# Kernel tuning notes

Hardware: AMD Instinct MI355X
Metric: run time of the kernel (lower is better)

Reference implementation:

```python
import jax, jax.numpy as jnp
import numpy as np

B, N_LAT, N_PAT = 32, 64, 4096
DIM_LAT = DIM_PAT = DIM_ATTN = 192
H = 6
HD = DIM_ATTN // H  # 32
SCALE = HD ** -0.5


def setup_inputs() -> dict:
    key = jax.random.key(0)
    ks = jax.random.split(key, 8)
    s = lambda fan_in: 1.0 / np.sqrt(fan_in)
    return {
        "x_latents": jax.random.normal(ks[0], (B, N_LAT, DIM_LAT), jnp.float32),
        "x_patches": jax.random.normal(ks[1], (B, N_PAT, DIM_PAT), jnp.float32),
        # weights stored [in, out] (torch Linear applies x @ W.T; math identical)
        "W_rv_lat": jax.random.uniform(ks[2], (DIM_LAT, 2 * DIM_ATTN), jnp.float32, -s(DIM_LAT), s(DIM_LAT)),
        "W_rv_pat": jax.random.uniform(ks[3], (DIM_PAT, 2 * DIM_ATTN), jnp.float32, -s(DIM_PAT), s(DIM_PAT)),
        "W_proj_lat": jax.random.uniform(ks[4], (DIM_ATTN, DIM_LAT), jnp.float32, -s(DIM_ATTN), s(DIM_ATTN)),
        "b_proj_lat": jax.random.uniform(ks[5], (DIM_LAT,), jnp.float32, -s(DIM_ATTN), s(DIM_ATTN)),
        "W_proj_pat": jax.random.uniform(ks[6], (DIM_ATTN, DIM_PAT), jnp.float32, -s(DIM_ATTN), s(DIM_ATTN)),
        "b_proj_pat": jax.random.uniform(ks[7], (DIM_PAT,), jnp.float32, -s(DIM_ATTN), s(DIM_ATTN)),
    }


def _split_rv(x, W, n):
    # x: [B, n, d_in] -> r, v each [B, H, n, HD]
    rv = (x @ W).reshape(x.shape[0], n, 2, H, HD)
    rv = jnp.transpose(rv, (2, 0, 3, 1, 4))  # [2, B, H, n, HD]
    return rv[0], rv[1]


def reference(x_latents, x_patches, W_rv_lat, W_rv_pat,
              W_proj_lat, b_proj_lat, W_proj_pat, b_proj_pat):
    r_lat, v_lat = _split_rv(x_latents, W_rv_lat, N_LAT)   # [B,H,N_lat,HD]
    r_pat, v_pat = _split_rv(x_patches, W_rv_pat, N_PAT)   # [B,H,N_pat,HD]

    # single score matrix, softmaxed along both axes (dropout = 0, eval mode)
    scores = jnp.einsum('bhld,bhpd->bhlp', r_lat, r_pat) * SCALE  # [B,H,N_lat,N_pat]
    attn = jax.nn.softmax(scores, axis=-1)    # row-wise (over patches)
    attn_T = jax.nn.softmax(scores, axis=-2)  # col-wise (over latents)

    out_lat = jnp.einsum('bhlp,bhpd->blhd', attn, v_pat).reshape(B, N_LAT, DIM_ATTN)
    out_pat = jnp.einsum('bhlp,bhld->bphd', attn_T, v_lat).reshape(B, N_PAT, DIM_ATTN)

    out_lat = out_lat @ W_proj_lat + b_proj_lat
    out_pat = out_pat @ W_proj_pat + b_proj_pat
    return out_lat, out_pat
```

## Files before the change

kernel.cpp:

```cpp
#include <hip/hip_runtime.h>

#define B_   32
#define NL_  64
#define NP_  4096
#define DIM_ 192
#define H_   6
#define HD_  32
#define PC_  128
#define NCH_ (NP_/PC_)

typedef unsigned short u16;
typedef __attribute__((ext_vector_type(8))) short bf16x8;
typedef __attribute__((ext_vector_type(4))) short bf16x4;
typedef __attribute__((ext_vector_type(4))) float f32x4;

#define MFMA16(a,b,c) __builtin_amdgcn_mfma_f32_16x16x32_bf16(a,b,c,0,0,0)

__device__ __forceinline__ float bf2f(u16 s){ return __builtin_bit_cast(float,(unsigned)s<<16); }
__device__ __forceinline__ u16 f2bf(float f){
  unsigned u = __builtin_bit_cast(unsigned,f);
  return (u16)((u + 0x7FFFu + ((u>>16)&1u))>>16);
}

__global__ void k0_transpose(const float* __restrict__ W0, const float* __restrict__ W1,
                             const float* __restrict__ W2, const float* __restrict__ W3,
                             u16* __restrict__ T0, u16* __restrict__ T1,
                             u16* __restrict__ T2, u16* __restrict__ T3){
  int m = blockIdx.x >> 4, sub = blockIdx.x & 15;
  const float* src; u16* dst; int R, C;
  if      (m==0){src=W0;dst=T0;R=192;C=384;}
  else if (m==1){src=W1;dst=T1;R=192;C=384;}
  else if (m==2){src=W2;dst=T2;R=192;C=192;}
  else          {src=W3;dst=T3;R=192;C=192;}
  int total = R*C;
  for (int o = sub*256 + threadIdx.x; o < total; o += 16*256){
    int c = o / R, r = o - c*R;
    dst[o] = f2bf(src[r*C + c]);
  }
}

__global__ __launch_bounds__(256) void k_rv(const float* __restrict__ X,
    const u16* __restrict__ Wt, u16* __restrict__ R, u16* __restrict__ V,
    int Nseq, int nshift){
  __shared__ u16 As[64*200];
  __shared__ u16 Bs[64*200];
  const int t = threadIdx.x;
  const int m0 = blockIdx.x*64;
  const int lane = t & 63, w = t >> 6, g = lane >> 4, ln = lane & 15;
  const int wr = w >> 1, wc = w & 1;
  const int srow = t >> 2, sc = (t & 3) * 8;
  const f32x4 ZF = {0.f,0.f,0.f,0.f};

  #pragma unroll
  for (int k0 = 0; k0 < 192; k0 += 32){
    float4 x0 = *(const float4*)&X[(size_t)(m0 + srow)*192 + k0 + sc];
    float4 x1 = *(const float4*)&X[(size_t)(m0 + srow)*192 + k0 + sc + 4];
    bf16x8 av;
    av[0]=(short)f2bf(x0.x); av[1]=(short)f2bf(x0.y); av[2]=(short)f2bf(x0.z); av[3]=(short)f2bf(x0.w);
    av[4]=(short)f2bf(x1.x); av[5]=(short)f2bf(x1.y); av[6]=(short)f2bf(x1.z); av[7]=(short)f2bf(x1.w);
    *(bf16x8*)&As[srow*200 + k0 + sc] = av;
  }

  for (int n0 = 0; n0 < 384; n0 += 64){
    __syncthreads();
    #pragma unroll
    for (int k0 = 0; k0 < 192; k0 += 32)
      *(bf16x8*)&Bs[srow*200 + k0 + sc] = *(const bf16x8*)&Wt[(size_t)(n0 + srow)*192 + k0 + sc];
    __syncthreads();

    f32x4 acc[2][2];
    #pragma unroll
    for(int i=0;i<2;i++){ acc[i][0]=ZF; acc[i][1]=ZF; }
    #pragma unroll
    for (int k0 = 0; k0 < 192; k0 += 32){
      bf16x8 a0 = *(const bf16x8*)&As[(wr*32      + ln)*200 + k0 + g*8];
      bf16x8 a1 = *(const bf16x8*)&As[(wr*32 + 16 + ln)*200 + k0 + g*8];
      bf16x8 b0 = *(const bf16x8*)&Bs[(wc*32      + ln)*200 + k0 + g*8];
      bf16x8 b1 = *(const bf16x8*)&Bs[(wc*32 + 16 + ln)*200 + k0 + g*8];
      acc[0][0] = MFMA16(a0,b0,acc[0][0]);
      acc[0][1] = MFMA16(a0,b1,acc[0][1]);
      acc[1][0] = MFMA16(a1,b0,acc[1][0]);
      acc[1][1] = MFMA16(a1,b1,acc[1][1]);
    }
    #pragma unroll
    for(int i=0;i<2;i++)
      #pragma unroll
      for(int j=0;j<2;j++){
        int n = n0 + wc*32 + j*16 + ln;
        u16* dst; int c;
        if (n < 192){ dst = R; c = n; } else { dst = V; c = n - 192; }
        int h = c >> 5, d = c & 31;
        #pragma unroll
        for(int r=0;r<4;r++){
          int m = m0 + wr*32 + i*16 + g*4 + r;
          int b = m >> nshift, sidx = m & (Nseq-1);
          dst[((((size_t)b*H_ + h)*(size_t)Nseq + sidx) << 5) + d] = f2bf(acc[i][j][r]);
        }
      }
  }
}

__global__ __launch_bounds__(256) void k_attn(
    const u16* __restrict__ r_lat_g, const u16* __restrict__ v_lat_g,
    const u16* __restrict__ r_pat_g, const u16* __restrict__ v_pat_g,
    u16* __restrict__ Opat,
    float* __restrict__ numT_ws,
    float* __restrict__ rowsum_ws){
  const float SCALE = 0.17677669529663687f;
  const int ci = blockIdx.x, h = blockIdx.y, b = blockIdx.z;
  const int bh = b*H_ + h;
  const int t = threadIdx.x, lane = t&63, w = t>>6, g = lane>>4, ln = lane&15;
  __shared__ u16 RL [64*40];
  __shared__ u16 VLT[32*72];
  __shared__ u16 EN [128*72];
  __shared__ u16 ET [64*136];
  __shared__ float RS[4*64];
  __shared__ u16 POOL[128*40];
  u16* RP  = POOL;
  u16* VPT = POOL;
  const f32x4 ZF = {0.f,0.f,0.f,0.f};

  const size_t latbase = (size_t)bh * (NL_*HD_);
  { int row = t>>2, col = (t&3)*8;
    *(bf16x8*)&RL[row*40+col] = *(const bf16x8*)&r_lat_g[latbase + row*32 + col]; }
  { int l = t>>2, dd = (t&3)*8;
    bf16x8 v = *(const bf16x8*)&v_lat_g[latbase + l*32 + dd];
    #pragma unroll
    for(int jj=0;jj<8;jj++) VLT[(dd+jj)*72 + l] = (u16)v[jj]; }
  const size_t patbase = ((size_t)bh*NP_ + (size_t)ci*PC_)*HD_;
  u16 vstash[16];
  #pragma unroll
  for(int it=0; it<2; it++){
    int p = it*64 + (t>>2), dd = (t&3)*8;
    *(bf16x8*)&RP[p*40+dd] = *(const bf16x8*)&r_pat_g[patbase + (size_t)p*32 + dd];
    bf16x8 vv = *(const bf16x8*)&v_pat_g[patbase + (size_t)p*32 + dd];
    #pragma unroll
    for(int jj=0;jj<8;jj++) vstash[it*8+jj] = (u16)vv[jj];
  }
  __syncthreads();

  f32x4 sf[2][4];
  { bf16x8 a[2], bl[4];
    #pragma unroll
    for(int i=0;i<2;i++) a[i]  = *(const bf16x8*)&RP[(w*32 + i*16 + ln)*40 + g*8];
    #pragma unroll
    for(int j=0;j<4;j++) bl[j] = *(const bf16x8*)&RL[(j*16 + ln)*40 + g*8];
    #pragma unroll
    for(int i=0;i<2;i++)
      #pragma unroll
      for(int j=0;j<4;j++) sf[i][j] = MFMA16(a[i], bl[j], ZF);
  }
  float e[2][4][4], rs[4] = {0.f,0.f,0.f,0.f};
  float rcs[2][4];
  #pragma unroll
  for(int i=0;i<2;i++)
    #pragma unroll
    for(int r=0;r<4;r++){
      float c = 0.f;
      #pragma unroll
      for(int j=0;j<4;j++){
        float ev = __expf(sf[i][j][r] * SCALE);
        e[i][j][r] = ev; c += ev; rs[j] += ev;
      }
      c += __shfl_xor(c,1); c += __shfl_xor(c,2);
      c += __shfl_xor(c,4); c += __shfl_xor(c,8);
      rcs[i][r] = 1.0f / c;
    }
  #pragma unroll
  for(int j=0;j<4;j++){
    float vs = rs[j];
    vs += __shfl_xor(vs,16); vs += __shfl_xor(vs,32);
    if (g == 0) RS[w*64 + j*16 + ln] = vs;
  }
  #pragma unroll
  for(int i=0;i<2;i++)
    #pragma unroll
    for(int j=0;j<4;j++){
      #pragma unroll
      for(int r=0;r<4;r++)
        EN[(w*32 + i*16 + g*4 + r)*72 + j*16 + ln] = f2bf(e[i][j][r]*rcs[i][r]);
      bf16x4 pk;
      #pragma unroll
      for(int r=0;r<4;r++) pk[r] = (short)f2bf(e[i][j][r]);
      *(bf16x4*)&ET[(j*16+ln)*136 + w*32 + i*16 + g*4] = pk;
    }
  __syncthreads();

  #pragma unroll
  for(int it=0; it<2; it++){
    int p = it*64 + (t>>2), dd = (t&3)*8;
    #pragma unroll
    for(int jj=0;jj<8;jj++) VPT[(dd+jj)*136 + p] = vstash[it*8+jj];
  }

  f32x4 op[2][2];
  #pragma unroll
  for(int i=0;i<2;i++){ op[i][0]=ZF; op[i][1]=ZF; }
  #pragma unroll
  for(int ks=0; ks<2; ks++){
    bf16x8 bv[2];
    #pragma unroll
    for(int jd=0;jd<2;jd++) bv[jd] = *(const bf16x8*)&VLT[(jd*16+ln)*72 + ks*32 + g*8];
    #pragma unroll
    for(int i=0;i<2;i++){
      bf16x8 af = *(const bf16x8*)&EN[(w*32 + i*16 + ln)*72 + ks*32 + g*8];
      #pragma unroll
      for(int jd=0;jd<2;jd++) op[i][jd] = MFMA16(af, bv[jd], op[i][jd]);
    }
  }
  const size_t obase = ((size_t)b*NP_ + (size_t)ci*PC_)*DIM_ + h*32;
  #pragma unroll
  for(int i=0;i<2;i++)
    #pragma unroll
    for(int jd=0;jd<2;jd++)
      #pragma unroll
      for(int r=0;r<4;r++){
        int p = w*32 + i*16 + g*4 + r, dd = jd*16 + ln;
        Opat[obase + (size_t)p*DIM_ + dd] = f2bf(op[i][jd][r]);
      }
  __syncthreads();

  f32x4 nm[2]; nm[0]=ZF; nm[1]=ZF;
  #pragma unroll
  for(int ks=0; ks<4; ks++){
    bf16x8 af = *(const bf16x8*)&ET[(w*16+ln)*136 + ks*32 + g*8];
    #pragma unroll
    for(int dj=0;dj<2;dj++){
      bf16x8 bv = *(const bf16x8*)&VPT[(dj*16+ln)*136 + ks*32 + g*8];
      nm[dj] = MFMA16(af, bv, nm[dj]);
    }
  }
  float* dstN = numT_ws + ((size_t)bh*NCH_ + ci)*2048;
  #pragma unroll
  for(int dj=0;dj<2;dj++)
    #pragma unroll
    for(int r=0;r<4;r++){
      int l = w*16 + g*4 + r, dd = dj*16 + ln;
      dstN[l*32 + dd] = nm[dj][r];
    }
  if (t < 64){
    float s = RS[t] + RS[64+t] + RS[128+t] + RS[192+t];
    rowsum_ws[((size_t)bh*NCH_ + ci)*64 + t] = s;
  }
}

__global__ __launch_bounds__(256) void k_lat_reduce(const float* __restrict__ numT_ws,
    const float* __restrict__ rowsum_ws, u16* __restrict__ attn_lat){
  int bh = blockIdx.x, b = bh / H_, h = bh - b*H_;
  __shared__ float RSs[64];
  int t = threadIdx.x;
  if (t < 64){
    float s = 0.f;
    for(int c=0;c<NCH_;c++) s += rowsum_ws[((size_t)bh*NCH_ + c)*64 + t];
    RSs[t] = 1.0f / s;
  }
  __syncthreads();
  for(int idx = t; idx < 2048; idx += 256){
    int l = idx >> 5, dd = idx & 31;
    float s = 0.f;
    for(int c=0;c<NCH_;c++) s += numT_ws[((size_t)bh*NCH_ + c)*2048 + idx];
    attn_lat[((size_t)b*NL_ + l)*DIM_ + h*32 + dd] = f2bf(s * RSs[l]);
  }
}

__global__ __launch_bounds__(256) void k_proj_lat(const u16* __restrict__ A,
    const u16* __restrict__ Wt, const float* __restrict__ bias, float* __restrict__ out){
  int b = blockIdx.x;
  __shared__ u16 As[64*40];
  __shared__ u16 Bs[192*40];
  int t = threadIdx.x, lane = t&63, w = t>>6, g = lane>>4, ln = lane&15;
  const f32x4 ZF = {0.f,0.f,0.f,0.f};
  f32x4 acc[4][3];
  #pragma unroll
  for(int i=0;i<4;i++)
    #pragma unroll
    for(int j=0;j<3;j++) acc[i][j]=ZF;
  for(int k0=0;k0<192;k0+=32){
    bf16x8 av; bf16x8 bv[3];
    { int row = t>>2, col=(t&3)*8;
      av = *(const bf16x8*)&A[((size_t)b*NL_ + row)*DIM_ + k0 + col]; }
    #pragma unroll
    for(int it=0;it<3;it++){
      int e = it*2048 + t*8, row = e>>5, col = (t&3)*8;
      bv[it] = *(const bf16x8*)&Wt[(size_t)row*192 + k0 + col];
    }
    if (k0) __syncthreads();
    { int row = t>>2, col=(t&3)*8; *(bf16x8*)&As[row*40+col] = av; }
    #pragma unroll
    for(int it=0;it<3;it++){
      int e = it*2048 + t*8, row = e>>5, col = (t&3)*8;
      *(bf16x8*)&Bs[row*40+col] = bv[it];
    }
    __syncthreads();
    bf16x8 bw[3];
    #pragma unroll
    for(int jf=0;jf<3;jf++) bw[jf] = *(const bf16x8*)&Bs[(w*48 + jf*16 + ln)*40 + g*8];
    #pragma unroll
    for(int lf=0;lf<4;lf++){
      bf16x8 af = *(const bf16x8*)&As[(lf*16 + ln)*40 + g*8];
      #pragma unroll
      for(int jf=0;jf<3;jf++) acc[lf][jf] = MFMA16(af, bw[jf], acc[lf][jf]);
    }
  }
  #pragma unroll
  for(int lf=0;lf<4;lf++)
    #pragma unroll
    for(int jf=0;jf<3;jf++){
      int j = w*48 + jf*16 + ln;
      float bs = bias[j];
      #pragma unroll
      for(int r=0;r<4;r++){
        int l = lf*16 + g*4 + r;
        out[((size_t)b*NL_ + l)*DIM_ + j] = acc[lf][jf][r] + bs;
      }
    }
}

__global__ __launch_bounds__(256) void k_proj_pat(const u16* __restrict__ X,
    const u16* __restrict__ Wt, const float* __restrict__ bias, float* __restrict__ out){
  __shared__ u16 As[64*40];
  __shared__ u16 Bs[64*40];
  const int t = threadIdx.x;
  const int m0 = blockIdx.x*64, n0 = blockIdx.y*64;
  const int lane = t & 63, w = t >> 6, g = lane >> 4, ln = lane & 15;
  const int wr = w >> 1, wc = w & 1;
  const int srow = t >> 2, scol = (t & 3) * 8;
  const f32x4 ZF = {0.f,0.f,0.f,0.f};
  f32x4 acc[2][2];
  #pragma unroll
  for(int i=0;i<2;i++){ acc[i][0]=ZF; acc[i][1]=ZF; }
  for (int k0 = 0; k0 < 192; k0 += 32){
    bf16x8 av = *(const bf16x8*)&X [(size_t)(m0 + srow)*192 + k0 + scol];
    bf16x8 bv = *(const bf16x8*)&Wt[(size_t)(n0 + srow)*192 + k0 + scol];
    if (k0) __syncthreads();
    *(bf16x8*)&As[srow*40 + scol] = av;
    *(bf16x8*)&Bs[srow*40 + scol] = bv;
    __syncthreads();
    bf16x8 a0 = *(const bf16x8*)&As[(wr*32      + ln)*40 + g*8];
    bf16x8 a1 = *(const bf16x8*)&As[(wr*32 + 16 + ln)*40 + g*8];
    bf16x8 b0 = *(const bf16x8*)&Bs[(wc*32      + ln)*40 + g*8];
    bf16x8 b1 = *(const bf16x8*)&Bs[(wc*32 + 16 + ln)*40 + g*8];
    acc[0][0] = MFMA16(a0,b0,acc[0][0]);
    acc[0][1] = MFMA16(a0,b1,acc[0][1]);
    acc[1][0] = MFMA16(a1,b0,acc[1][0]);
    acc[1][1] = MFMA16(a1,b1,acc[1][1]);
  }
  #pragma unroll
  for(int i=0;i<2;i++)
    #pragma unroll
    for(int j=0;j<2;j++){
      int n = n0 + wc*32 + j*16 + ln;
      float bs = bias[n];
      #pragma unroll
      for(int r=0;r<4;r++){
        int m = m0 + wr*32 + i*16 + g*4 + r;
        out[(size_t)m*192 + n] = acc[i][j][r] + bs;
      }
    }
}

extern "C" void kernel_launch(void* const* d_in, const int* in_sizes, int n_in,
                              void* d_out, int out_size, void* d_ws, size_t ws_size,
                              hipStream_t stream){
  const float* x_lat  = (const float*)d_in[0];
  const float* x_pat  = (const float*)d_in[1];
  const float* W_rv_l = (const float*)d_in[2];
  const float* W_rv_p = (const float*)d_in[3];
  const float* W_pj_l = (const float*)d_in[4];
  const float* b_pj_l = (const float*)d_in[5];
  const float* W_pj_p = (const float*)d_in[6];
  const float* b_pj_p = (const float*)d_in[7];
  float* out = (float*)d_out;

  char* ws = (char*)d_ws;
  size_t off = 0;
  auto alloc = [&](size_t bytes)->void*{ void* p = ws + off; off += (bytes + 255) & ~(size_t)255; return p; };
  u16* WtRL   = (u16*)alloc((size_t)384*192*2);
  u16* WtRP   = (u16*)alloc((size_t)384*192*2);
  u16* WtPL   = (u16*)alloc((size_t)192*192*2);
  u16* WtPP   = (u16*)alloc((size_t)192*192*2);
  u16* r_lat  = (u16*)alloc((size_t)B_*H_*NL_*HD_*2);
  u16* v_lat  = (u16*)alloc((size_t)B_*H_*NL_*HD_*2);
  u16* r_pat  = (u16*)alloc((size_t)B_*H_*NP_*HD_*2);
  u16* v_pat  = (u16*)alloc((size_t)B_*H_*NP_*HD_*2);
  u16* Opat   = (u16*)alloc((size_t)B_*NP_*DIM_*2);
  float* numT = (float*)alloc((size_t)B_*H_*NCH_*64*32*4);
  float* rsum = (float*)alloc((size_t)B_*H_*NCH_*64*4);
  u16* attn_l = (u16*)alloc((size_t)B_*NL_*DIM_*2);

  k0_transpose<<<64,256,0,stream>>>(W_rv_l, W_rv_p, W_pj_l, W_pj_p, WtRL, WtRP, WtPL, WtPP);
  k_rv<<<dim3((B_*NP_)/64),256,0,stream>>>(x_pat, WtRP, r_pat, v_pat, NP_, 12);
  k_rv<<<dim3((B_*NL_)/64),256,0,stream>>>(x_lat, WtRL, r_lat, v_lat, NL_, 6);
  k_attn<<<dim3(NCH_, H_, B_),256,0,stream>>>(r_lat, v_lat, r_pat, v_pat, Opat, numT, rsum);
  k_lat_reduce<<<B_*H_,256,0,stream>>>(numT, rsum, attn_l);
  k_proj_lat<<<B_,256,0,stream>>>(attn_l, WtPL, b_pj_l, out);
  k_proj_pat<<<dim3((B_*NP_)/64, 3),256,0,stream>>>(Opat, WtPP, b_pj_p, out + (size_t)B_*NL_*DIM_);
}
```

Before: 199.7 us.

## Fuse patch output projection into attention kernel and enlarge rv GEMM tiles

The attention kernel now loops over all six heads per block and accumulates the patch output projection in registers, writing final fp32 output with bias directly. This removes the bf16 Opat intermediate and the separate k_proj_pat launch. The rv projection kernel also processes 128 rows per block with 4x wider per-warp tiles and register-prefetches the next weight tile. The cost is fewer attention blocks (1024 instead of 6144), 96 accumulator registers per thread, and weight reads from global memory inside the head loop.

Result: slower. 233.5 us (+16.9%).

```diff
diff --git a/kernel.cpp b/kernel.cpp
--- a/kernel.cpp
+++ b/kernel.cpp
@@ -42,57 +42,75 @@
 __global__ __launch_bounds__(256) void k_rv(const float* __restrict__ X,
     const u16* __restrict__ Wt, u16* __restrict__ R, u16* __restrict__ V,
     int Nseq, int nshift){
-  __shared__ u16 As[64*200];
+  __shared__ u16 As[128*200];
   __shared__ u16 Bs[64*200];
   const int t = threadIdx.x;
-  const int m0 = blockIdx.x*64;
+  const int m0 = blockIdx.x*128;
   const int lane = t & 63, w = t >> 6, g = lane >> 4, ln = lane & 15;
-  const int wr = w >> 1, wc = w & 1;
   const int srow = t >> 2, sc = (t & 3) * 8;
+  const int bq = t & 3;
   const f32x4 ZF = {0.f,0.f,0.f,0.f};
 
   #pragma unroll
-  for (int k0 = 0; k0 < 192; k0 += 32){
-    float4 x0 = *(const float4*)&X[(size_t)(m0 + srow)*192 + k0 + sc];
-    float4 x1 = *(const float4*)&X[(size_t)(m0 + srow)*192 + k0 + sc + 4];
-    bf16x8 av;
-    av[0]=(short)f2bf(x0.x); av[1]=(short)f2bf(x0.y); av[2]=(short)f2bf(x0.z); av[3]=(short)f2bf(x0.w);
-    av[4]=(short)f2bf(x1.x); av[5]=(short)f2bf(x1.y); av[6]=(short)f2bf(x1.z); av[7]=(short)f2bf(x1.w);
-    *(bf16x8*)&As[srow*200 + k0 + sc] = av;
-  }
+  for (int rr = 0; rr < 128; rr += 64){
+    #pragma unroll
+    for (int k0 = 0; k0 < 192; k0 += 32){
+      float4 x0 = *(const float4*)&X[(size_t)(m0 + rr + srow)*192 + k0 + sc];
+      float4 x1 = *(const float4*)&X[(size_t)(m0 + rr + srow)*192 + k0 + sc + 4];
+      bf16x8 av;
+      av[0]=(short)f2bf(x0.x); av[1]=(short)f2bf(x0.y); av[2]=(short)f2bf(x0.z); av[3]=(short)f2bf(x0.w);
+      av[4]=(short)f2bf(x1.x); av[5]=(short)f2bf(x1.y); av[6]=(short)f2bf(x1.z); av[7]=(short)f2bf(x1.w);
+      *(bf16x8*)&As[(rr + srow)*200 + k0 + sc] = av;
+    }
+  }
+
+  bf16x8 breg[6];
+  #pragma unroll
+  for (int it=0; it<6; it++)
+    breg[it] = *(const bf16x8*)&Wt[(size_t)srow*192 + bq*48 + it*8];
+
+  __syncthreads();
 
   for (int n0 = 0; n0 < 384; n0 += 64){
-    __syncthreads();
-    #pragma unroll
-    for (int k0 = 0; k0 < 192; k0 += 32)
-      *(bf16x8*)&Bs[srow*200 + k0 + sc] = *(const bf16x8*)&Wt[(size_t)(n0 + srow)*192 + k0 + sc];
-    __syncthreads();
-
-    f32x4 acc[2][2];
-    #pragma unroll
-    for(int i=0;i<2;i++){ acc[i][0]=ZF; acc[i][1]=ZF; }
+    #pragma unroll
+    for (int it=0; it<6; it++)
+      *(bf16x8*)&Bs[srow*200 + bq*48 + it*8] = breg[it];
+    if (n0 < 320){
+      #pragma unroll
+      for (int it=0; it<6; it++)
+        breg[it] = *(const bf16x8*)&Wt[(size_t)(n0 + 64 + srow)*192 + bq*48 + it*8];
+    }
+    __syncthreads();
+
+    f32x4 acc[2][4];
+    #pragma unroll
+    for(int i=0;i<2;i++)
+      #pragma unroll
+      for(int j=0;j<4;j++) acc[i][j]=ZF;
     #pragma unroll
     for (int k0 = 0; k0 < 192; k0 += 32){
-      bf16x8 a0 = *(const bf16x8*)&As[(wr*32      + ln)*200 + k0 + g*8];
-      bf16x8 a1 = *(const bf16x8*)&As[(wr*32 + 16 + ln)*200 + k0 + g*8];
-      bf16x8 b0 = *(const bf16x8*)&Bs[(wc*32      + ln)*200 + k0 + g*8];
-      bf16x8 b1 = *(const bf16x8*)&Bs[(wc*32 + 16 + ln)*200 + k0 + g*8];
-      acc[0][0] = MFMA16(a0,b0,acc[0][0]);
-      acc[0][1] = MFMA16(a0,b1,acc[0][1]);
-      acc[1][0] = MFMA16(a1,b0,acc[1][0]);
-      acc[1][1] = MFMA16(a1,b1,acc[1][1]);
-    }
-    #pragma unroll
-    for(int i=0;i<2;i++)
-      #pragma unroll
-      for(int j=0;j<2;j++){
-        int n = n0 + wc*32 + j*16 + ln;
+      bf16x8 a0 = *(const bf16x8*)&As[(w*32      + ln)*200 + k0 + g*8];
+      bf16x8 a1 = *(const bf16x8*)&As[(w*32 + 16 + ln)*200 + k0 + g*8];
+      #pragma unroll
+      for(int j=0;j<4;j++){
+        bf16x8 bv = *(const bf16x8*)&Bs[(j*16 + ln)*200 + k0 + g*8];
+        acc[0][j] = MFMA16(a0,bv,acc[0][j]);
+        acc[1][j] = MFMA16(a1,bv,acc[1][j]);
+      }
+    }
+    __syncthreads();
+
+    #pragma unroll
+    for(int i=0;i<2;i++)
+      #pragma unroll
+      for(int j=0;j<4;j++){
+        int n = n0 + j*16 + ln;
         u16* dst; int c;
         if (n < 192){ dst = R; c = n; } else { dst = V; c = n - 192; }
         int h = c >> 5, d = c & 31;
         #pragma unroll
         for(int r=0;r<4;r++){
-          int m = m0 + wr*32 + i*16 + g*4 + r;
+          int m = m0 + w*32 + i*16 + g*4 + r;
           int b = m >> nshift, sidx = m & (Nseq-1);
           dst[((((size_t)b*H_ + h)*(size_t)Nseq + sidx) << 5) + d] = f2bf(acc[i][j][r]);
         }
@@ -103,12 +121,13 @@
 __global__ __launch_bounds__(256) void k_attn(
     const u16* __restrict__ r_lat_g, const u16* __restrict__ v_lat_g,
     const u16* __restrict__ r_pat_g, const u16* __restrict__ v_pat_g,
-    u16* __restrict__ Opat,
+    const u16* __restrict__ Wpt,
+    const float* __restrict__ bias,
+    float* __restrict__ outp,
     float* __restrict__ numT_ws,
     float* __restrict__ rowsum_ws){
   const float SCALE = 0.17677669529663687f;
-  const int ci = blockIdx.x, h = blockIdx.y, b = blockIdx.z;
-  const int bh = b*H_ + h;
+  const int ci = blockIdx.x, b = blockIdx.y;
   const int t = threadIdx.x, lane = t&63, w = t>>6, g = lane>>4, ln = lane&15;
   __shared__ u16 RL [64*40];
   __shared__ u16 VLT[32*72];
@@ -118,129 +137,161 @@
   __shared__ u16 POOL[128*40];
   u16* RP  = POOL;
   u16* VPT = POOL;
+  u16* PRE = ET;
   const f32x4 ZF = {0.f,0.f,0.f,0.f};
 
-  const size_t latbase = (size_t)bh * (NL_*HD_);
-  { int row = t>>2, col = (t&3)*8;
-    *(bf16x8*)&RL[row*40+col] = *(const bf16x8*)&r_lat_g[latbase + row*32 + col]; }
-  { int l = t>>2, dd = (t&3)*8;
-    bf16x8 v = *(const bf16x8*)&v_lat_g[latbase + l*32 + dd];
-    #pragma unroll
-    for(int jj=0;jj<8;jj++) VLT[(dd+jj)*72 + l] = (u16)v[jj]; }
-  const size_t patbase = ((size_t)bh*NP_ + (size_t)ci*PC_)*HD_;
-  u16 vstash[16];
-  #pragma unroll
-  for(int it=0; it<2; it++){
-    int p = it*64 + (t>>2), dd = (t&3)*8;
-    *(bf16x8*)&RP[p*40+dd] = *(const bf16x8*)&r_pat_g[patbase + (size_t)p*32 + dd];
-    bf16x8 vv = *(const bf16x8*)&v_pat_g[patbase + (size_t)p*32 + dd];
-    #pragma unroll
-    for(int jj=0;jj<8;jj++) vstash[it*8+jj] = (u16)vv[jj];
-  }
-  __syncthreads();
-
-  f32x4 sf[2][4];
-  { bf16x8 a[2], bl[4];
-    #pragma unroll
-    for(int i=0;i<2;i++) a[i]  = *(const bf16x8*)&RP[(w*32 + i*16 + ln)*40 + g*8];
-    #pragma unroll
-    for(int j=0;j<4;j++) bl[j] = *(const bf16x8*)&RL[(j*16 + ln)*40 + g*8];
-    #pragma unroll
-    for(int i=0;i<2;i++)
-      #pragma unroll
-      for(int j=0;j<4;j++) sf[i][j] = MFMA16(a[i], bl[j], ZF);
-  }
-  float e[2][4][4], rs[4] = {0.f,0.f,0.f,0.f};
-  float rcs[2][4];
+  f32x4 pacc[2][12];
   #pragma unroll
   for(int i=0;i<2;i++)
     #pragma unroll
-    for(int r=0;r<4;r++){
-      float c = 0.f;
+    for(int jc=0;jc<12;jc++) pacc[i][jc]=ZF;
+
+  for (int h = 0; h < H_; ++h){
+    const int bh = b*H_ + h;
+    const size_t latbase = (size_t)bh * (NL_*HD_);
+    const size_t patbase = ((size_t)bh*NP_ + (size_t)ci*PC_)*HD_;
+
+    { int row = t>>2, col = (t&3)*8;
+      *(bf16x8*)&RL[row*40+col] = *(const bf16x8*)&r_lat_g[latbase + row*32 + col]; }
+    { int l = t>>2, dd = (t&3)*8;
+      bf16x8 v = *(const bf16x8*)&v_lat_g[latbase + l*32 + dd];
+      #pragma unroll
+      for(int jj=0;jj<8;jj++) VLT[(dd+jj)*72 + l] = (u16)v[jj]; }
+    u16 vstash[16];
+    #pragma unroll
+    for(int it=0; it<2; it++){
+      int p = it*64 + (t>>2), dd = (t&3)*8;
+      *(bf16x8*)&RP[p*40+dd] = *(const bf16x8*)&r_pat_g[patbase + (size_t)p*32 + dd];
+      bf16x8 vv = *(const bf16x8*)&v_pat_g[patbase + (size_t)p*32 + dd];
+      #pragma unroll
+      for(int jj=0;jj<8;jj++) vstash[it*8+jj] = (u16)vv[jj];
+    }
+    __syncthreads();
+
+    f32x4 sf[2][4];
+    { bf16x8 a[2], bl[4];
+      #pragma unroll
+      for(int i=0;i<2;i++) a[i]  = *(const bf16x8*)&RP[(w*32 + i*16 + ln)*40 + g*8];
+      #pragma unroll
+      for(int j=0;j<4;j++) bl[j] = *(const bf16x8*)&RL[(j*16 + ln)*40 + g*8];
+      #pragma unroll
+      for(int i=0;i<2;i++)
+        #pragma unroll
+        for(int j=0;j<4;j++) sf[i][j] = MFMA16(a[i], bl[j], ZF);
+    }
+    float e[2][4][4], rs[4] = {0.f,0.f,0.f,0.f};
+    float rcs[2][4];
+    #pragma unroll
+    for(int i=0;i<2;i++)
+      #pragma unroll
+      for(int r=0;r<4;r++){
+        float c = 0.f;
+        #pragma unroll
+        for(int j=0;j<4;j++){
+          float ev = __expf(sf[i][j][r] * SCALE);
+          e[i][j][r] = ev; c += ev; rs[j] += ev;
+        }
+        c += __shfl_xor(c,1); c += __shfl_xor(c,2);
+        c += __shfl_xor(c,4); c += __shfl_xor(c,8);
+        rcs[i][r] = 1.0f / c;
+      }
+    #pragma unroll
+    for(int j=0;j<4;j++){
+      float vs = rs[j];
+      vs += __shfl_xor(vs,16); vs += __shfl_xor(vs,32);
+      if (g == 0) RS[w*64 + j*16 + ln] = vs;
+    }
+    #pragma unroll
+    for(int i=0;i<2;i++)
       #pragma unroll
       for(int j=0;j<4;j++){
-        float ev = __expf(sf[i][j][r] * SCALE);
-        e[i][j][r] = ev; c += ev; rs[j] += ev;
-      }
-      c += __shfl_xor(c,1); c += __shfl_xor(c,2);
-      c += __shfl_xor(c,4); c += __shfl_xor(c,8);
-      rcs[i][r] = 1.0f / c;
-    }
-  #pragma unroll
-  for(int j=0;j<4;j++){
-    float vs = rs[j];
-    vs += __shfl_xor(vs,16); vs += __shfl_xor(vs,32);
-    if (g == 0) RS[w*64 + j*16 + ln] = vs;
-  }
-  #pragma unroll
-  for(int i=0;i<2;i++)
-    #pragma unroll
-    for(int j=0;j<4;j++){
-      #pragma unroll
-      for(int r=0;r<4;r++)
-        EN[(w*32 + i*16 + g*4 + r)*72 + j*16 + ln] = f2bf(e[i][j][r]*rcs[i][r]);
-      bf16x4 pk;
-      #pragma unroll
-      for(int r=0;r<4;r++) pk[r] = (short)f2bf(e[i][j][r]);
-      *(bf16x4*)&ET[(j*16+ln)*136 + w*32 + i*16 + g*4] = pk;
-    }
-  __syncthreads();
-
-  #pragma unroll
-  for(int it=0; it<2; it++){
-    int p = it*64 + (t>>2), dd = (t&3)*8;
-    #pragma unroll
-    for(int jj=0;jj<8;jj++) VPT[(dd+jj)*136 + p] = vstash[it*8+jj];
-  }
-
-  f32x4 op[2][2];
-  #pragma unroll
-  for(int i=0;i<2;i++){ op[i][0]=ZF; op[i][1]=ZF; }
-  #pragma unroll
-  for(int ks=0; ks<2; ks++){
-    bf16x8 bv[2];
-    #pragma unroll
-    for(int jd=0;jd<2;jd++) bv[jd] = *(const bf16x8*)&VLT[(jd*16+ln)*72 + ks*32 + g*8];
-    #pragma unroll
-    for(int i=0;i<2;i++){
-      bf16x8 af = *(const bf16x8*)&EN[(w*32 + i*16 + ln)*72 + ks*32 + g*8];
-      #pragma unroll
-      for(int jd=0;jd<2;jd++) op[i][jd] = MFMA16(af, bv[jd], op[i][jd]);
-    }
-  }
-  const size_t obase = ((size_t)b*NP_ + (size_t)ci*PC_)*DIM_ + h*32;
-  #pragma unroll
-  for(int i=0;i<2;i++)
-    #pragma unroll
-    for(int jd=0;jd<2;jd++)
+        #pragma unroll
+        for(int r=0;r<4;r++)
+          EN[(w*32 + i*16 + g*4 + r)*72 + j*16 + ln] = f2bf(e[i][j][r]*rcs[i][r]);
+        bf16x4 pk;
+        #pragma unroll
+        for(int r=0;r<4;r++) pk[r] = (short)f2bf(e[i][j][r]);
+        *(bf16x4*)&ET[(j*16+ln)*136 + w*32 + i*16 + g*4] = pk;
+      }
+    __syncthreads();
+
+    #pragma unroll
+    for(int it=0; it<2; it++){
+      int p = it*64 + (t>>2), dd = (t&3)*8;
+      #pragma unroll
+      for(int jj=0;jj<8;jj++) VPT[(dd+jj)*136 + p] = vstash[it*8+jj];
+    }
+
+    f32x4 op[2][2];
+    #pragma unroll
+    for(int i=0;i<2;i++){ op[i][0]=ZF; op[i][1]=ZF; }
+    #pragma unroll
+    for(int ks=0; ks<2; ks++){
+      bf16x8 bv[2];
+      #pragma unroll
+      for(int jd=0;jd<2;jd++) bv[jd] = *(const bf16x8*)&VLT[(jd*16+ln)*72 + ks*32 + g*8];
+      #pragma unroll
+      for(int i=0;i<2;i++){
+        bf16x8 af = *(const bf16x8*)&EN[(w*32 + i*16 + ln)*72 + ks*32 + g*8];
+        #pragma unroll
+        for(int jd=0;jd<2;jd++) op[i][jd] = MFMA16(af, bv[jd], op[i][jd]);
+      }
+    }
+    __syncthreads();
+
+    f32x4 nm[2]; nm[0]=ZF; nm[1]=ZF;
+    #pragma unroll
+    for(int ks=0; ks<4; ks++){
+      bf16x8 af = *(const bf16x8*)&ET[(w*16+ln)*136 + ks*32 + g*8];
+      #pragma unroll
+      for(int dj=0;dj<2;dj++){
+        bf16x8 bv = *(const bf16x8*)&VPT[(dj*16+ln)*136 + ks*32 + g*8];
+        nm[dj] = MFMA16(af, bv, nm[dj]);
+      }
+    }
+    float* dstN = numT_ws + ((size_t)bh*NCH_ + ci)*2048;
+    #pragma unroll
+    for(int dj=0;dj<2;dj++)
       #pragma unroll
       for(int r=0;r<4;r++){
-        int p = w*32 + i*16 + g*4 + r, dd = jd*16 + ln;
-        Opat[obase + (size_t)p*DIM_ + dd] = f2bf(op[i][jd][r]);
-      }
-  __syncthreads();
-
-  f32x4 nm[2]; nm[0]=ZF; nm[1]=ZF;
-  #pragma unroll
-  for(int ks=0; ks<4; ks++){
-    bf16x8 af = *(const bf16x8*)&ET[(w*16+ln)*136 + ks*32 + g*8];
-    #pragma unroll
-    for(int dj=0;dj<2;dj++){
-      bf16x8 bv = *(const bf16x8*)&VPT[(dj*16+ln)*136 + ks*32 + g*8];
-      nm[dj] = MFMA16(af, bv, nm[dj]);
-    }
-  }
-  float* dstN = numT_ws + ((size_t)bh*NCH_ + ci)*2048;
-  #pragma unroll
-  for(int dj=0;dj<2;dj++)
-    #pragma unroll
-    for(int r=0;r<4;r++){
-      int l = w*16 + g*4 + r, dd = dj*16 + ln;
-      dstN[l*32 + dd] = nm[dj][r];
-    }
-  if (t < 64){
-    float s = RS[t] + RS[64+t] + RS[128+t] + RS[192+t];
-    rowsum_ws[((size_t)bh*NCH_ + ci)*64 + t] = s;
+        int l = w*16 + g*4 + r, dd = dj*16 + ln;
+        dstN[l*32 + dd] = nm[dj][r];
+      }
+    if (t < 64){
+      float s = RS[t] + RS[64+t] + RS[128+t] + RS[192+t];
+      rowsum_ws[((size_t)bh*NCH_ + ci)*64 + t] = s;
+    }
+    __syncthreads();
+
+    #pragma unroll
+    for(int i=0;i<2;i++)
+      #pragma unroll
+      for(int jd=0;jd<2;jd++)
+        #pragma unroll
+        for(int r=0;r<4;r++)
+          PRE[(w*32 + i*16 + g*4 + r)*40 + jd*16 + ln] = f2bf(op[i][jd][r]);
+    bf16x8 pa[2];
+    #pragma unroll
+    for(int i=0;i<2;i++) pa[i] = *(const bf16x8*)&PRE[(w*32 + i*16 + ln)*40 + g*8];
+    #pragma unroll
+    for(int jc=0;jc<12;jc++){
+      bf16x8 wb = *(const bf16x8*)&Wpt[(size_t)(jc*16+ln)*192 + h*32 + g*8];
+      pacc[0][jc] = MFMA16(pa[0], wb, pacc[0][jc]);
+      pacc[1][jc] = MFMA16(pa[1], wb, pacc[1][jc]);
+    }
+  }
+
+  const size_t obase = ((size_t)b*NP_ + (size_t)ci*PC_)*DIM_;
+  #pragma unroll
+  for(int jc=0;jc<12;jc++){
+    float bs = bias[jc*16+ln];
+    #pragma unroll
+    for(int i=0;i<2;i++)
+      #pragma unroll
+      for(int r=0;r<4;r++){
+        int p = w*32 + i*16 + g*4 + r;
+        outp[obase + (size_t)p*DIM_ + jc*16 + ln] = pacc[i][jc][r] + bs;
+      }
   }
 }
 
@@ -312,49 +363,6 @@
       for(int r=0;r<4;r++){
         int l = lf*16 + g*4 + r;
         out[((size_t)b*NL_ + l)*DIM_ + j] = acc[lf][jf][r] + bs;
-      }
-    }
-}
-
-__global__ __launch_bounds__(256) void k_proj_pat(const u16* __restrict__ X,
-    const u16* __restrict__ Wt, const float* __restrict__ bias, float* __restrict__ out){
-  __shared__ u16 As[64*40];
-  __shared__ u16 Bs[64*40];
-  const int t = threadIdx.x;
-  const int m0 = blockIdx.x*64, n0 = blockIdx.y*64;
-  const int lane = t & 63, w = t >> 6, g = lane >> 4, ln = lane & 15;
-  const int wr = w >> 1, wc = w & 1;
-  const int srow = t >> 2, scol = (t & 3) * 8;
-  const f32x4 ZF = {0.f,0.f,0.f,0.f};
-  f32x4 acc[2][2];
-  #pragma unroll
-  for(int i=0;i<2;i++){ acc[i][0]=ZF; acc[i][1]=ZF; }
-  for (int k0 = 0; k0 < 192; k0 += 32){
-    bf16x8 av = *(const bf16x8*)&X [(size_t)(m0 + srow)*192 + k0 + scol];
-    bf16x8 bv = *(const bf16x8*)&Wt[(size_t)(n0 + srow)*192 + k0 + scol];
-    if (k0) __syncthreads();
-    *(bf16x8*)&As[srow*40 + scol] = av;
-    *(bf16x8*)&Bs[srow*40 + scol] = bv;
-    __syncthreads();
-    bf16x8 a0 = *(const bf16x8*)&As[(wr*32      + ln)*40 + g*8];
-    bf16x8 a1 = *(const bf16x8*)&As[(wr*32 + 16 + ln)*40 + g*8];
-    bf16x8 b0 = *(const bf16x8*)&Bs[(wc*32      + ln)*40 + g*8];
-    bf16x8 b1 = *(const bf16x8*)&Bs[(wc*32 + 16 + ln)*40 + g*8];
-    acc[0][0] = MFMA16(a0,b0,acc[0][0]);
-    acc[0][1] = MFMA16(a0,b1,acc[0][1]);
-    acc[1][0] = MFMA16(a1,b0,acc[1][0]);
-    acc[1][1] = MFMA16(a1,b1,acc[1][1]);
-  }
-  #pragma unroll
-  for(int i=0;i<2;i++)
-    #pragma unroll
-    for(int j=0;j<2;j++){
-      int n = n0 + wc*32 + j*16 + ln;
-      float bs = bias[n];
-      #pragma unroll
-      for(int r=0;r<4;r++){
-        int m = m0 + wr*32 + i*16 + g*4 + r;
-        out[(size_t)m*192 + n] = acc[i][j][r] + bs;
       }
     }
 }
@@ -383,16 +391,15 @@
   u16* v_lat  = (u16*)alloc((size_t)B_*H_*NL_*HD_*2);
   u16* r_pat  = (u16*)alloc((size_t)B_*H_*NP_*HD_*2);
   u16* v_pat  = (u16*)alloc((size_t)B_*H_*NP_*HD_*2);
-  u16* Opat   = (u16*)alloc((size_t)B_*NP_*DIM_*2);
   float* numT = (float*)alloc((size_t)B_*H_*NCH_*64*32*4);
   float* rsum = (float*)alloc((size_t)B_*H_*NCH_*64*4);
   u16* attn_l = (u16*)alloc((size_t)B_*NL_*DIM_*2);
 
   k0_transpose<<<64,256,0,stream>>>(W_rv_l, W_rv_p, W_pj_l, W_pj_p, WtRL, WtRP, WtPL, WtPP);
-  k_rv<<<dim3((B_*NP_)/64),256,0,stream>>>(x_pat, WtRP, r_pat, v_pat, NP_, 12);
-  k_rv<<<dim3((B_*NL_)/64),256,0,stream>>>(x_lat, WtRL, r_lat, v_lat, NL_, 6);
-  k_attn<<<dim3(NCH_, H_, B_),256,0,stream>>>(r_lat, v_lat, r_pat, v_pat, Opat, numT, rsum);
+  k_rv<<<dim3((B_*NP_)/128),256,0,stream>>>(x_pat, WtRP, r_pat, v_pat, NP_, 12);
+  k_rv<<<dim3((B_*NL_)/128),256,0,stream>>>(x_lat, WtRL, r_lat, v_lat, NL_, 6);
+  k_attn<<<dim3(NCH_, B_),256,0,stream>>>(r_lat, v_lat, r_pat, v_pat, WtPP, b_pj_p,
+                                          out + (size_t)B_*NL_*DIM_, numT, rsum);
   k_lat_reduce<<<B_*H_,256,0,stream>>>(numT, rsum, attn_l);
   k_proj_lat<<<B_,256,0,stream>>>(attn_l, WtPL, b_pj_l, out);
-  k_proj_pat<<<dim3((B_*NP_)/64, 3),256,0,stream>>>(Opat, WtPP, b_pj_p, out + (size_t)B_*NL_*DIM_);
-}
+}
```

## Enlarge projection tiles, prefetch weights, and loop attention over four patch chunks

Applied to the files above, without the earlier changes.

The rv projection kernel now processes 128 rows per block, with each wave computing a full 64-column strip, and it prefetches the next weight tile into registers while the current one is consumed. The attention kernel now loops over four 128-patch chunks per block. It accumulates the latent numerator and rowsum in registers and prefetches the next chunk's r/v, which cuts the workspace partials and the reduce work by four. The cost is fewer blocks in flight, more registers, and more LDS per k_rv block. For the latent call, (32*64)/128 = 16 blocks still covers all rows exactly.

New measurement: 190.0 us. -4.9%, faster.

```diff
diff --git a/kernel.cpp b/kernel.cpp
--- a/kernel.cpp
+++ b/kernel.cpp
@@ -8,6 +8,8 @@
 #define HD_  32
 #define PC_  128
 #define NCH_ (NP_/PC_)
+#define CPB_ 4
+#define NSC_ (NCH_/CPB_)
 
 typedef unsigned short u16;
 typedef __attribute__((ext_vector_type(8))) short bf16x8;
@@ -42,57 +44,75 @@
 __global__ __launch_bounds__(256) void k_rv(const float* __restrict__ X,
     const u16* __restrict__ Wt, u16* __restrict__ R, u16* __restrict__ V,
     int Nseq, int nshift){
-  __shared__ u16 As[64*200];
+  __shared__ u16 As[128*200];
   __shared__ u16 Bs[64*200];
   const int t = threadIdx.x;
-  const int m0 = blockIdx.x*64;
+  const int m0 = blockIdx.x*128;
   const int lane = t & 63, w = t >> 6, g = lane >> 4, ln = lane & 15;
-  const int wr = w >> 1, wc = w & 1;
   const int srow = t >> 2, sc = (t & 3) * 8;
+  const int bq = t & 3;
   const f32x4 ZF = {0.f,0.f,0.f,0.f};
 
   #pragma unroll
-  for (int k0 = 0; k0 < 192; k0 += 32){
-    float4 x0 = *(const float4*)&X[(size_t)(m0 + srow)*192 + k0 + sc];
-    float4 x1 = *(const float4*)&X[(size_t)(m0 + srow)*192 + k0 + sc + 4];
-    bf16x8 av;
-    av[0]=(short)f2bf(x0.x); av[1]=(short)f2bf(x0.y); av[2]=(short)f2bf(x0.z); av[3]=(short)f2bf(x0.w);
-    av[4]=(short)f2bf(x1.x); av[5]=(short)f2bf(x1.y); av[6]=(short)f2bf(x1.z); av[7]=(short)f2bf(x1.w);
-    *(bf16x8*)&As[srow*200 + k0 + sc] = av;
-  }
+  for (int rr = 0; rr < 128; rr += 64){
+    #pragma unroll
+    for (int k0 = 0; k0 < 192; k0 += 32){
+      float4 x0 = *(const float4*)&X[(size_t)(m0 + rr + srow)*192 + k0 + sc];
+      float4 x1 = *(const float4*)&X[(size_t)(m0 + rr + srow)*192 + k0 + sc + 4];
+      bf16x8 av;
+      av[0]=(short)f2bf(x0.x); av[1]=(short)f2bf(x0.y); av[2]=(short)f2bf(x0.z); av[3]=(short)f2bf(x0.w);
+      av[4]=(short)f2bf(x1.x); av[5]=(short)f2bf(x1.y); av[6]=(short)f2bf(x1.z); av[7]=(short)f2bf(x1.w);
+      *(bf16x8*)&As[(rr + srow)*200 + k0 + sc] = av;
+    }
+  }
+
+  bf16x8 breg[6];
+  #pragma unroll
+  for (int it=0; it<6; it++)
+    breg[it] = *(const bf16x8*)&Wt[(size_t)srow*192 + bq*48 + it*8];
+
+  __syncthreads();
 
   for (int n0 = 0; n0 < 384; n0 += 64){
-    __syncthreads();
-    #pragma unroll
-    for (int k0 = 0; k0 < 192; k0 += 32)
-      *(bf16x8*)&Bs[srow*200 + k0 + sc] = *(const bf16x8*)&Wt[(size_t)(n0 + srow)*192 + k0 + sc];
-    __syncthreads();
-
-    f32x4 acc[2][2];
-    #pragma unroll
-    for(int i=0;i<2;i++){ acc[i][0]=ZF; acc[i][1]=ZF; }
+    #pragma unroll
+    for (int it=0; it<6; it++)
+      *(bf16x8*)&Bs[srow*200 + bq*48 + it*8] = breg[it];
+    if (n0 < 320){
+      #pragma unroll
+      for (int it=0; it<6; it++)
+        breg[it] = *(const bf16x8*)&Wt[(size_t)(n0 + 64 + srow)*192 + bq*48 + it*8];
+    }
+    __syncthreads();
+
+    f32x4 acc[2][4];
+    #pragma unroll
+    for(int i=0;i<2;i++)
+      #pragma unroll
+      for(int j=0;j<4;j++) acc[i][j]=ZF;
     #pragma unroll
     for (int k0 = 0; k0 < 192; k0 += 32){
-      bf16x8 a0 = *(const bf16x8*)&As[(wr*32      + ln)*200 + k0 + g*8];
-      bf16x8 a1 = *(const bf16x8*)&As[(wr*32 + 16 + ln)*200 + k0 + g*8];
-      bf16x8 b0 = *(const bf16x8*)&Bs[(wc*32      + ln)*200 + k0 + g*8];
-      bf16x8 b1 = *(const bf16x8*)&Bs[(wc*32 + 16 + ln)*200 + k0 + g*8];
-      acc[0][0] = MFMA16(a0,b0,acc[0][0]);
-      acc[0][1] = MFMA16(a0,b1,acc[0][1]);
-      acc[1][0] = MFMA16(a1,b0,acc[1][0]);
-      acc[1][1] = MFMA16(a1,b1,acc[1][1]);
-    }
+      bf16x8 a0 = *(const bf16x8*)&As[(w*32      + ln)*200 + k0 + g*8];
+      bf16x8 a1 = *(const bf16x8*)&As[(w*32 + 16 + ln)*200 + k0 + g*8];
+      #pragma unroll
+      for(int j=0;j<4;j++){
+        bf16x8 bv = *(const bf16x8*)&Bs[(j*16 + ln)*200 + k0 + g*8];
+        acc[0][j] = MFMA16(a0,bv,acc[0][j]);
+        acc[1][j] = MFMA16(a1,bv,acc[1][j]);
+      }
+    }
+    __syncthreads();
+
     #pragma unroll
     for(int i=0;i<2;i++)
       #pragma unroll
-      for(int j=0;j<2;j++){
-        int n = n0 + wc*32 + j*16 + ln;
+      for(int j=0;j<4;j++){
+        int n = n0 + j*16 + ln;
         u16* dst; int c;
         if (n < 192){ dst = R; c = n; } else { dst = V; c = n - 192; }
         int h = c >> 5, d = c & 31;
         #pragma unroll
         for(int r=0;r<4;r++){
-          int m = m0 + wr*32 + i*16 + g*4 + r;
+          int m = m0 + w*32 + i*16 + g*4 + r;
           int b = m >> nshift, sidx = m & (Nseq-1);
           dst[((((size_t)b*H_ + h)*(size_t)Nseq + sidx) << 5) + d] = f2bf(acc[i][j][r]);
         }
@@ -107,7 +127,7 @@
     float* __restrict__ numT_ws,
     float* __restrict__ rowsum_ws){
   const float SCALE = 0.17677669529663687f;
-  const int ci = blockIdx.x, h = blockIdx.y, b = blockIdx.z;
+  const int sc = blockIdx.x, h = blockIdx.y, b = blockIdx.z;
   const int bh = b*H_ + h;
   const int t = threadIdx.x, lane = t&63, w = t>>6, g = lane>>4, ln = lane&15;
   __shared__ u16 RL [64*40];
@@ -127,110 +147,128 @@
     bf16x8 v = *(const bf16x8*)&v_lat_g[latbase + l*32 + dd];
     #pragma unroll
     for(int jj=0;jj<8;jj++) VLT[(dd+jj)*72 + l] = (u16)v[jj]; }
-  const size_t patbase = ((size_t)bh*NP_ + (size_t)ci*PC_)*HD_;
-  u16 vstash[16];
-  #pragma unroll
-  for(int it=0; it<2; it++){
-    int p = it*64 + (t>>2), dd = (t&3)*8;
-    *(bf16x8*)&RP[p*40+dd] = *(const bf16x8*)&r_pat_g[patbase + (size_t)p*32 + dd];
-    bf16x8 vv = *(const bf16x8*)&v_pat_g[patbase + (size_t)p*32 + dd];
-    #pragma unroll
-    for(int jj=0;jj<8;jj++) vstash[it*8+jj] = (u16)vv[jj];
-  }
-  __syncthreads();
-
-  f32x4 sf[2][4];
-  { bf16x8 a[2], bl[4];
-    #pragma unroll
-    for(int i=0;i<2;i++) a[i]  = *(const bf16x8*)&RP[(w*32 + i*16 + ln)*40 + g*8];
-    #pragma unroll
-    for(int j=0;j<4;j++) bl[j] = *(const bf16x8*)&RL[(j*16 + ln)*40 + g*8];
+
+  const int p0 = t>>2, dd0 = (t&3)*8;
+  const size_t pb0 = ((size_t)bh*NP_ + (size_t)sc*(CPB_*PC_))*HD_;
+  bf16x8 rcur0 = *(const bf16x8*)&r_pat_g[pb0 + (size_t)p0*32 + dd0];
+  bf16x8 rcur1 = *(const bf16x8*)&r_pat_g[pb0 + (size_t)(64+p0)*32 + dd0];
+  bf16x8 vcur0 = *(const bf16x8*)&v_pat_g[pb0 + (size_t)p0*32 + dd0];
+  bf16x8 vcur1 = *(const bf16x8*)&v_pat_g[pb0 + (size_t)(64+p0)*32 + dd0];
+
+  f32x4 nm[2]; nm[0]=ZF; nm[1]=ZF;
+  float rs[4] = {0.f,0.f,0.f,0.f};
+
+  for (int c = 0; c < CPB_; ++c){
+    *(bf16x8*)&RP[p0*40 + dd0]      = rcur0;
+    *(bf16x8*)&RP[(64+p0)*40 + dd0] = rcur1;
+    __syncthreads();
+
+    f32x4 sf[2][4];
+    { bf16x8 a0 = *(const bf16x8*)&RP[(w*32      + ln)*40 + g*8];
+      bf16x8 a1 = *(const bf16x8*)&RP[(w*32 + 16 + ln)*40 + g*8];
+      #pragma unroll
+      for(int j=0;j<4;j++){
+        bf16x8 bl = *(const bf16x8*)&RL[(j*16 + ln)*40 + g*8];
+        sf[0][j] = MFMA16(a0, bl, ZF);
+        sf[1][j] = MFMA16(a1, bl, ZF);
+      } }
+
+    bf16x8 rnxt0, rnxt1, vnxt0, vnxt1;
+    const bool more = (c+1 < CPB_);
+    if (more){
+      const size_t pbn = pb0 + (size_t)(c+1)*(PC_*HD_);
+      rnxt0 = *(const bf16x8*)&r_pat_g[pbn + (size_t)p0*32 + dd0];
+      rnxt1 = *(const bf16x8*)&r_pat_g[pbn + (size_t)(64+p0)*32 + dd0];
+      vnxt0 = *(const bf16x8*)&v_pat_g[pbn + (size_t)p0*32 + dd0];
+      vnxt1 = *(const bf16x8*)&v_pat_g[pbn + (size_t)(64+p0)*32 + dd0];
+    }
+
+    float e[2][4][4], rcs[2][4];
     #pragma unroll
     for(int i=0;i<2;i++)
       #pragma unroll
-      for(int j=0;j<4;j++) sf[i][j] = MFMA16(a[i], bl[j], ZF);
-  }
-  float e[2][4][4], rs[4] = {0.f,0.f,0.f,0.f};
-  float rcs[2][4];
-  #pragma unroll
-  for(int i=0;i<2;i++)
-    #pragma unroll
-    for(int r=0;r<4;r++){
-      float c = 0.f;
+      for(int r=0;r<4;r++){
+        float cs = 0.f;
+        #pragma unroll
+        for(int j=0;j<4;j++){
+          float ev = __expf(sf[i][j][r] * SCALE);
+          e[i][j][r] = ev; cs += ev; rs[j] += ev;
+        }
+        cs += __shfl_xor(cs,1); cs += __shfl_xor(cs,2);
+        cs += __shfl_xor(cs,4); cs += __shfl_xor(cs,8);
+        rcs[i][r] = 1.0f / cs;
+      }
+    #pragma unroll
+    for(int i=0;i<2;i++)
       #pragma unroll
       for(int j=0;j<4;j++){
-        float ev = __expf(sf[i][j][r] * SCALE);
-        e[i][j][r] = ev; c += ev; rs[j] += ev;
-      }
-      c += __shfl_xor(c,1); c += __shfl_xor(c,2);
-      c += __shfl_xor(c,4); c += __shfl_xor(c,8);
-      rcs[i][r] = 1.0f / c;
-    }
+        #pragma unroll
+        for(int r=0;r<4;r++)
+          EN[(w*32 + i*16 + g*4 + r)*72 + j*16 + ln] = f2bf(e[i][j][r]*rcs[i][r]);
+        bf16x4 pk;
+        #pragma unroll
+        for(int r=0;r<4;r++) pk[r] = (short)f2bf(e[i][j][r]);
+        *(bf16x4*)&ET[(j*16+ln)*136 + w*32 + i*16 + g*4] = pk;
+      }
+    __syncthreads();
+
+    #pragma unroll
+    for(int jj=0;jj<8;jj++){
+      VPT[(dd0+jj)*136 + p0]      = (u16)vcur0[jj];
+      VPT[(dd0+jj)*136 + 64 + p0] = (u16)vcur1[jj];
+    }
+
+    f32x4 op[2][2];
+    #pragma unroll
+    for(int i=0;i<2;i++){ op[i][0]=ZF; op[i][1]=ZF; }
+    #pragma unroll
+    for(int ks=0; ks<2; ks++){
+      bf16x8 bv[2];
+      #pragma unroll
+      for(int jd=0;jd<2;jd++) bv[jd] = *(const bf16x8*)&VLT[(jd*16+ln)*72 + ks*32 + g*8];
+      #pragma unroll
+      for(int i=0;i<2;i++){
+        bf16x8 af = *(const bf16x8*)&EN[(w*32 + i*16 + ln)*72 + ks*32 + g*8];
+        #pragma unroll
+        for(int jd=0;jd<2;jd++) op[i][jd] = MFMA16(af, bv[jd], op[i][jd]);
+      }
+    }
+    const size_t obase = ((size_t)b*NP_ + (size_t)(sc*CPB_ + c)*PC_)*DIM_ + h*32;
+    #pragma unroll
+    for(int i=0;i<2;i++)
+      #pragma unroll
+      for(int jd=0;jd<2;jd++)
+        #pragma unroll
+        for(int r=0;r<4;r++){
+          int p = w*32 + i*16 + g*4 + r, dd = jd*16 + ln;
+          Opat[obase + (size_t)p*DIM_ + dd] = f2bf(op[i][jd][r]);
+        }
+    __syncthreads();
+
+    #pragma unroll
+    for(int ks=0; ks<4; ks++){
+      bf16x8 af = *(const bf16x8*)&ET[(w*16+ln)*136 + ks*32 + g*8];
+      #pragma unroll
+      for(int dj=0;dj<2;dj++){
+        bf16x8 bv = *(const bf16x8*)&VPT[(dj*16+ln)*136 + ks*32 + g*8];
+        nm[dj] = MFMA16(af, bv, nm[dj]);
+      }
+    }
+    __syncthreads();
+
+    if (more){ rcur0=rnxt0; rcur1=rnxt1; vcur0=vnxt0; vcur1=vnxt1; }
+  }
+
   #pragma unroll
   for(int j=0;j<4;j++){
     float vs = rs[j];
     vs += __shfl_xor(vs,16); vs += __shfl_xor(vs,32);
     if (g == 0) RS[w*64 + j*16 + ln] = vs;
   }
-  #pragma unroll
-  for(int i=0;i<2;i++)
-    #pragma unroll
-    for(int j=0;j<4;j++){
-      #pragma unroll
-      for(int r=0;r<4;r++)
-        EN[(w*32 + i*16 + g*4 + r)*72 + j*16 + ln] = f2bf(e[i][j][r]*rcs[i][r]);
-      bf16x4 pk;
-      #pragma unroll
-      for(int r=0;r<4;r++) pk[r] = (short)f2bf(e[i][j][r]);
-      *(bf16x4*)&ET[(j*16+ln)*136 + w*32 + i*16 + g*4] = pk;
-    }
   __syncthreads();
-
-  #pragma unroll
-  for(int it=0; it<2; it++){
-    int p = it*64 + (t>>2), dd = (t&3)*8;
-    #pragma unroll
-    for(int jj=0;jj<8;jj++) VPT[(dd+jj)*136 + p] = vstash[it*8+jj];
-  }
-
-  f32x4 op[2][2];
-  #pragma unroll
-  for(int i=0;i<2;i++){ op[i][0]=ZF; op[i][1]=ZF; }
-  #pragma unroll
-  for(int ks=0; ks<2; ks++){
-    bf16x8 bv[2];
-    #pragma unroll
-    for(int jd=0;jd<2;jd++) bv[jd] = *(const bf16x8*)&VLT[(jd*16+ln)*72 + ks*32 + g*8];
-    #pragma unroll
-    for(int i=0;i<2;i++){
-      bf16x8 af = *(const bf16x8*)&EN[(w*32 + i*16 + ln)*72 + ks*32 + g*8];
-      #pragma unroll
-      for(int jd=0;jd<2;jd++) op[i][jd] = MFMA16(af, bv[jd], op[i][jd]);
-    }
-  }
-  const size_t obase = ((size_t)b*NP_ + (size_t)ci*PC_)*DIM_ + h*32;
-  #pragma unroll
-  for(int i=0;i<2;i++)
-    #pragma unroll
-    for(int jd=0;jd<2;jd++)
-      #pragma unroll
-      for(int r=0;r<4;r++){
-        int p = w*32 + i*16 + g*4 + r, dd = jd*16 + ln;
-        Opat[obase + (size_t)p*DIM_ + dd] = f2bf(op[i][jd][r]);
-      }
-  __syncthreads();
-
-  f32x4 nm[2]; nm[0]=ZF; nm[1]=ZF;
-  #pragma unroll
-  for(int ks=0; ks<4; ks++){
-    bf16x8 af = *(const bf16x8*)&ET[(w*16+ln)*136 + ks*32 + g*8];
-    #pragma unroll
-    for(int dj=0;dj<2;dj++){
-      bf16x8 bv = *(const bf16x8*)&VPT[(dj*16+ln)*136 + ks*32 + g*8];
-      nm[dj] = MFMA16(af, bv, nm[dj]);
-    }
-  }
-  float* dstN = numT_ws + ((size_t)bh*NCH_ + ci)*2048;
+  if (t < 64)
+    rowsum_ws[((size_t)bh*NSC_ + sc)*64 + t] = RS[t] + RS[64+t] + RS[128+t] + RS[192+t];
+  float* dstN = numT_ws + ((size_t)bh*NSC_ + sc)*2048;
   #pragma unroll
   for(int dj=0;dj<2;dj++)
     #pragma unroll
@@ -238,10 +276,6 @@
       int l = w*16 + g*4 + r, dd = dj*16 + ln;
       dstN[l*32 + dd] = nm[dj][r];
     }
-  if (t < 64){
-    float s = RS[t] + RS[64+t] + RS[128+t] + RS[192+t];
-    rowsum_ws[((size_t)bh*NCH_ + ci)*64 + t] = s;
-  }
 }
 
 __global__ __launch_bounds__(256) void k_lat_reduce(const float* __restrict__ numT_ws,
@@ -251,14 +285,14 @@
   int t = threadIdx.x;
   if (t < 64){
     float s = 0.f;
-    for(int c=0;c<NCH_;c++) s += rowsum_ws[((size_t)bh*NCH_ + c)*64 + t];
+    for(int c=0;c<NSC_;c++) s += rowsum_ws[((size_t)bh*NSC_ + c)*64 + t];
     RSs[t] = 1.0f / s;
   }
   __syncthreads();
   for(int idx = t; idx < 2048; idx += 256){
     int l = idx >> 5, dd = idx & 31;
     float s = 0.f;
-    for(int c=0;c<NCH_;c++) s += numT_ws[((size_t)bh*NCH_ + c)*2048 + idx];
+    for(int c=0;c<NSC_;c++) s += numT_ws[((size_t)bh*NSC_ + c)*2048 + idx];
     attn_lat[((size_t)b*NL_ + l)*DIM_ + h*32 + dd] = f2bf(s * RSs[l]);
   }
 }
@@ -384,14 +418,14 @@
   u16* r_pat  = (u16*)alloc((size_t)B_*H_*NP_*HD_*2);
   u16* v_pat  = (u16*)alloc((size_t)B_*H_*NP_*HD_*2);
   u16* Opat   = (u16*)alloc((size_t)B_*NP_*DIM_*2);
-  float* numT = (float*)alloc((size_t)B_*H_*NCH_*64*32*4);
-  float* rsum = (float*)alloc((size_t)B_*H_*NCH_*64*4);
+  float* numT = (float*)alloc((size_t)B_*H_*NSC_*64*32*4);
+  float* rsum = (float*)alloc((size_t)B_*H_*NSC_*64*4);
   u16* attn_l = (u16*)alloc((size_t)B_*NL_*DIM_*2);
 
   k0_transpose<<<64,256,0,stream>>>(W_rv_l, W_rv_p, W_pj_l, W_pj_p, WtRL, WtRP, WtPL, WtPP);
-  k_rv<<<dim3((B_*NP_)/64),256,0,stream>>>(x_pat, WtRP, r_pat, v_pat, NP_, 12);
-  k_rv<<<dim3((B_*NL_)/64),256,0,stream>>>(x_lat, WtRL, r_lat, v_lat, NL_, 6);
-  k_attn<<<dim3(NCH_, H_, B_),256,0,stream>>>(r_lat, v_lat, r_pat, v_pat, Opat, numT, rsum);
+  k_rv<<<dim3((B_*NP_)/128),256,0,stream>>>(x_pat, WtRP, r_pat, v_pat, NP_, 12);
+  k_rv<<<dim3((B_*NL_)/128),256,0,stream>>>(x_lat, WtRL, r_lat, v_lat, NL_, 6);
+  k_attn<<<dim3(NSC_, H_, B_),256,0,stream>>>(r_lat, v_lat, r_pat, v_pat, Opat, numT, rsum);
   k_lat_reduce<<<B_*H_,256,0,stream>>>(numT, rsum, attn_l);
   k_proj_lat<<<B_,256,0,stream>>>(attn_l, WtPL, b_pj_l, out);
   k_proj_pat<<<dim3((B_*NP_)/64, 3),256,0,stream>>>(Opat, WtPP, b_pj_p, out + (size_t)B_*NL_*DIM_);
```
